# Kernel optimization log

Hardware: AMD Instinct MI355X
Metric: run time of the kernel (lower is better)

Reference implementation:

```python
import jax, jax.numpy as jnp
import numpy as np

B, S, NC, ND, V = 16, 512, 10000, 10000, 128


def _rn(k, shape, scale=0.05):
    return jax.random.normal(k, shape, dtype=jnp.float32) * scale


def setup_inputs() -> dict:
    key = jax.random.key(0)
    ks = jax.random.split(key, 24)
    inp = {
        'c_seq': jax.random.randint(ks[0], (B, S), 0, NC),
        'd_seq': jax.random.randint(ks[1], (B, S), 0, ND),
        'r_seq': jax.random.uniform(ks[2], (B, S), dtype=jnp.float32),
        # embeddings / vectors
        'D1_w': _rn(ks[3], (ND, 1)),
        'D2_w': _rn(ks[4], (ND, V)),
        'v_r': _rn(ks[5], (V,)),
        'v_beta': _rn(ks[6], (V,)),
        # GRU (torch layout: gates ordered r,z,n; W_ih [3V,2V], W_hh [3V,V])
        'W_ih': _rn(ks[7], (3 * V, 2 * V)),
        'W_hh': _rn(ks[8], (3 * V, V)),
        'b_ih': jnp.zeros((3 * V,), jnp.float32),
        'b_hh': jnp.zeros((3 * V,), jnp.float32),
        # linear_1: V -> V -> V -> 1 (weights stored [in, out])
        'm1_W1': _rn(ks[9], (V, V)), 'm1_b1': jnp.zeros((V,), jnp.float32),
        'm1_W2': _rn(ks[10], (V, V)), 'm1_b2': jnp.zeros((V,), jnp.float32),
        'm1_W3': _rn(ks[11], (V, 1)), 'm1_b3': jnp.zeros((1,), jnp.float32),
        # linear_2: 3V -> V -> V -> 1
        'm2_W1': _rn(ks[12], (3 * V, V)), 'm2_b1': jnp.zeros((V,), jnp.float32),
        'm2_W2': _rn(ks[13], (V, V)), 'm2_b2': jnp.zeros((V,), jnp.float32),
        'm2_W3': _rn(ks[14], (V, 1)), 'm2_b3': jnp.zeros((1,), jnp.float32),
    }
    return inp


def _mlp(x, W1, b1, W2, b2, W3, b3):
    h = jax.nn.relu(x @ W1 + b1)
    h = jax.nn.relu(h @ W2 + b2)
    return h @ W3 + b3


def _gru_seq(x, W_ih, W_hh, b_ih, b_hh):
    # x: [B,S,2V] -> h_seq [B,S,V]; torch GRU gate order r,z,n
    xp = x @ W_ih.T + b_ih  # [B,S,3V]

    def step(h, xt):
        hp = h @ W_hh.T + b_hh
        xr, xz, xn = jnp.split(xt, 3, axis=-1)
        hr, hz, hn = jnp.split(hp, 3, axis=-1)
        r = jax.nn.sigmoid(xr + hr)
        z = jax.nn.sigmoid(xz + hz)
        n = jnp.tanh(xn + r * hn)
        h_new = (1.0 - z) * n + z * h
        return h_new, h_new

    h0 = jnp.zeros((x.shape[0], W_hh.shape[1]), x.dtype)
    _, hs = jax.lax.scan(step, h0, jnp.swapaxes(xp, 0, 1))  # [S,B,V]
    return jnp.swapaxes(hs, 0, 1)


def reference(c_seq, d_seq, r_seq, D1_w, D2_w, v_r, v_beta,
              W_ih, W_hh, b_ih, b_hh,
              m1_W1, m1_b1, m1_W2, m1_b2, m1_W3, m1_b3,
              m2_W1, m2_b1, m2_W2, m2_b2, m2_W3, m2_b3):
    v_d_seq = D2_w[d_seq]                     # [B,S,V]
    v_r_seq = r_seq[..., None] * v_r          # [B,S,V]

    h_seq = _gru_seq(jnp.concatenate([v_d_seq, v_r_seq], axis=-1),
                     W_ih, W_hh, b_ih, b_hh)  # [B,S,V]
    alpha_seq = _mlp(h_seq, m1_W1, m1_b1, m1_W2, m1_b2, m1_W3, m1_b3)[..., 0]  # [B,S]

    bidx = jnp.arange(c_seq.shape[0])

    def step(C, ins):
        c_t, vd_t, vr_t = ins                 # [B], [B,V], [B,V]
        beta_prev = C[bidx, c_t]              # gather: [B]
        v_beta_prev = beta_prev[:, None] * v_beta  # [B,V]
        new_c = _mlp(jnp.concatenate([v_beta_prev, vd_t, vr_t], axis=-1),
                     m2_W1, m2_b1, m2_W2, m2_b2, m2_W3, m2_b3)[:, 0]  # [B]
        C = C.at[bidx, c_t].set(new_c)        # scatter
        return C, (C, new_c)

    C0 = jnp.zeros((c_seq.shape[0], NC), jnp.float32)
    _, (C_seq, beta_seq) = jax.lax.scan(
        step, C0,
        (jnp.swapaxes(c_seq, 0, 1), jnp.swapaxes(v_d_seq, 0, 1), jnp.swapaxes(v_r_seq, 0, 1)))
    C_seq = jnp.swapaxes(C_seq, 0, 1)[..., None]   # [B,S,NC,1]
    beta_seq = jnp.swapaxes(beta_seq, 0, 1)        # [B,S]

    gamma_seq = D1_w[d_seq][..., 0]                # [B,S]
    return (alpha_seq, beta_seq, gamma_seq, h_seq, C_seq)
```

## Files before the change

### kernel.cpp

```cpp
#include <hip/hip_runtime.h>

#define Bq   16
#define Sq   512
#define Vq   128
#define NCq  10000

typedef __attribute__((ext_vector_type(8))) short short8v;
typedef __attribute__((ext_vector_type(4))) float f32x4;

#define OFF_P1B_U  3145728u
#define OFF_WTIH   2097152u
#define OFF_WVRIH  2146304u
#define OFF_WVR1   2146688u
#define OFF_WVB    2146816u
#define OFF_PO     2146944u

#define PLN 136
#define PLSZ (16*PLN+8)

__device__ __forceinline__ unsigned short f2bf(float x) {
    unsigned u = __builtin_bit_cast(unsigned, x);
    unsigned r = (u + 0x7fffu + ((u >> 16) & 1u)) >> 16;
    return (unsigned short)r;
}
__device__ __forceinline__ float bfhi(unsigned u) {
    return __builtin_bit_cast(float, u << 16);
}
__device__ __forceinline__ float bflo(unsigned u) {
    return __builtin_bit_cast(float, u & 0xffff0000u);
}
__device__ __forceinline__ void barrier_lgkm() {
    asm volatile("s_waitcnt lgkmcnt(0)" ::: "memory");
    __builtin_amdgcn_sched_barrier(0);
    __builtin_amdgcn_s_barrier();
    __builtin_amdgcn_sched_barrier(0);
}

__global__ __launch_bounds__(256) void k0_prep(
    const int* __restrict__ c_seq, const int* __restrict__ d_seq,
    const float* __restrict__ D1_w,
    const float* __restrict__ W_ih,
    const float* __restrict__ v_r, const float* __restrict__ v_beta,
    const float* __restrict__ m2W1,
    float* __restrict__ ws, float* __restrict__ gamma_out)
{
    const int blk = blockIdx.x, tid = threadIdx.x;

    if (blk < 128) {
        float* WTIH = ws + OFF_WTIH;
        int base = blk * 384;
        for (int i = tid; i < 384; i += 256) {
            int e = base + i;
            int k = e / 384, g = e % 384;
            WTIH[e] = W_ih[g * 256 + k];
        }
    } else if (blk == 128) {
        float* WVRIH = ws + OFF_WVRIH;
        float* WVR1  = ws + OFF_WVR1;
        float* WVB   = ws + OFF_WVB;
        for (int g = tid; g < 384; g += 256) {
            float a = 0.f;
            for (int k = 0; k < 128; ++k) a = fmaf(v_r[k], W_ih[g * 256 + 128 + k], a);
            WVRIH[g] = a;
        }
        if (tid < 128) {
            float a = 0.f, b = 0.f;
            for (int k = 0; k < 128; ++k) {
                a = fmaf(v_r[k],    m2W1[(256 + k) * 128 + tid], a);
                b = fmaf(v_beta[k], m2W1[k * 128 + tid],         b);
            }
            WVR1[tid] = a; WVB[tid] = b;
        }
    } else if (blk < 145) {
        const int b = blk - 129;
        __shared__ int cs[Sq];
        for (int i = tid; i < Sq; i += 256) cs[i] = c_seq[b * Sq + i];
        __syncthreads();
        int* PO = (int*)(ws + OFF_PO);
        for (int t = tid; t < Sq; t += 256) {
            int c = cs[t];
            int po = -1;
            for (int u = t - 1; u >= 0; --u) if (cs[u] == c) { po = u; break; }
            PO[t * 16 + b] = po;
        }
    } else {
        const int b = blk - 145;
        for (int s = tid; s < Sq; s += 256)
            gamma_out[b * Sq + s] = D1_w[d_seq[b * Sq + s]];
    }
}

__global__ __launch_bounds__(256) void k1_gemm(
    const int* __restrict__ d_seq, const float* __restrict__ D2_w,
    const float* __restrict__ m2W1,
    const float* __restrict__ b_ih, const float* __restrict__ b_hh,
    const float* __restrict__ r_seq, const float* __restrict__ m2b1,
    float* __restrict__ ws)
{
    __shared__ float As[64 * 128];
    __shared__ float Bs[128 * 64];
    const int blk = blockIdx.x, tid = threadIdx.x;
    const int nc = blk & 7;
    const int m0 = (blk >> 3) * 64;
    const float* WTIH = ws + OFF_WTIH;

    const float4* D2v = (const float4*)D2_w;
    for (int e = tid; e < 2048; e += 256) {
        int r = e >> 5, q = e & 31;
        int d = d_seq[m0 + r];
        *(float4*)&As[r * 128 + 4 * q] = D2v[d * 32 + q];
    }
    for (int e = tid; e < 2048; e += 256) {
        int k = e >> 4, q = e & 15;
        float4 v;
        if (nc < 6) v = *(const float4*)&WTIH[k * 384 + nc * 64 + 4 * q];
        else        v = *(const float4*)&m2W1[(128 + k) * 128 + (nc - 6) * 64 + 4 * q];
        *(float4*)&Bs[k * 64 + 4 * q] = v;
    }
    __syncthreads();

    const int tx = tid & 15, ty = tid >> 4;
    const int c0 = 4 * tx, r0 = 4 * ty;
    float acc[4][4];
#pragma unroll
    for (int i = 0; i < 4; ++i)
#pragma unroll
        for (int j = 0; j < 4; ++j) acc[i][j] = 0.f;

    for (int k = 0; k < 128; ++k) {
        float4 bv = *(const float4*)&Bs[k * 64 + c0];
#pragma unroll
        for (int i = 0; i < 4; ++i) {
            float a = As[(r0 + i) * 128 + k];
            acc[i][0] = fmaf(a, bv.x, acc[i][0]);
            acc[i][1] = fmaf(a, bv.y, acc[i][1]);
            acc[i][2] = fmaf(a, bv.z, acc[i][2]);
            acc[i][3] = fmaf(a, bv.w, acc[i][3]);
        }
    }

    float rsv[4];
#pragma unroll
    for (int i = 0; i < 4; ++i) rsv[i] = r_seq[m0 + r0 + i];

    if (nc < 6) {
        const int grow0 = nc * 64 + c0;
        float4 bi  = *(const float4*)&b_ih[grow0];
        float4 wv4 = *(const float4*)&(ws + OFF_WVRIH)[grow0];
        float4 bh4 = make_float4(0.f, 0.f, 0.f, 0.f);
        if (nc < 4) bh4 = *(const float4*)&b_hh[grow0];
        unsigned short* XPB = (unsigned short*)ws;
        const int r4 = grow0 >> 2;
#pragma unroll
        for (int i = 0; i < 4; ++i) {
            int row = m0 + r0 + i;
            int t = row & 511, bb = row >> 9;
            float vx = acc[i][0] + bi.x + bh4.x + rsv[i] * wv4.x;
            float vy = acc[i][1] + bi.y + bh4.y + rsv[i] * wv4.y;
            float vz = acc[i][2] + bi.z + bh4.z + rsv[i] * wv4.z;
            float vw = acc[i][3] + bi.w + bh4.w + rsv[i] * wv4.w;
            uint2 p;
            p.x = (unsigned)f2bf(vx) | ((unsigned)f2bf(vy) << 16);
            p.y = (unsigned)f2bf(vz) | ((unsigned)f2bf(vw) << 16);
            *(uint2*)&XPB[((size_t)((bb >> 2) * 512 + t)) * 1536 + r4 * 16 + (bb & 3) * 4] = p;
        }
    } else {
        const int j0 = (nc - 6) * 64 + c0;
        float4 b1v = *(const float4*)&m2b1[j0];
        float4 wr1 = *(const float4*)&(ws + OFF_WVR1)[j0];
        unsigned short* P1B = (unsigned short*)ws + OFF_P1B_U;
#pragma unroll
        for (int i = 0; i < 4; ++i) {
            int row = m0 + r0 + i;
            int t = row & 511, bb = row >> 9;
            float vx = acc[i][0] + b1v.x + rsv[i] * wr1.x;
            float vy = acc[i][1] + b1v.y + rsv[i] * wr1.y;
            float vz = acc[i][2] + b1v.z + rsv[i] * wr1.z;
            float vw = acc[i][3] + b1v.w + rsv[i] * wr1.w;
            uint2 p;
            p.x = (unsigned)f2bf(vx) | ((unsigned)f2bf(vy) << 16);
            p.y = (unsigned)f2bf(vz) | ((unsigned)f2bf(vw) << 16);
            *(uint2*)&P1B[((size_t)(t * 16 + bb)) * 128 + j0] = p;
        }
    }
}

__global__ __launch_bounds__(512, 1) void k2_scan(
    const float* __restrict__ W_hh, const float* __restrict__ b_hh,
    const float* __restrict__ m2W2, const float* __restrict__ m2b2,
    const float* __restrict__ m2W3, const float* __restrict__ m2b3,
    float* __restrict__ ws,
    float* __restrict__ hseq_out, float* __restrict__ beta_out)
{
    __shared__ __align__(16) unsigned char smem[12800];
    const int tid = threadIdx.x;
    const int l = tid & 63, wv = tid >> 6;
    const int qq = l >> 4, cb = l & 15;
    const int bgid = blockIdx.x;

    if (bgid < 4) {
        unsigned short* hP = (unsigned short*)smem;
        const unsigned short* XPB = (const unsigned short*)ws;

        short8v aH0[4], aH1[4], aH2[4];
#pragma unroll
        for (int kf = 0; kf < 4; ++kf) {
            const int kb = kf * 32 + qq * 8;
            const float* w0 = W_hh + (0 * 128 + 16 * wv + cb) * 128 + kb;
            const float* w1 = W_hh + (1 * 128 + 16 * wv + cb) * 128 + kb;
            const float* w2 = W_hh + (2 * 128 + 16 * wv + cb) * 128 + kb;
            short8v h0, h1, h2;
#pragma unroll
            for (int e = 0; e < 8; ++e) {
                h0[e] = (short)f2bf(w0[e]);
                h1[e] = (short)f2bf(w1[e]);
                h2[e] = (short)f2bf(w2[e]);
            }
            aH0[kf] = h0; aH1[kf] = h1; aH2[kf] = h2;
        }
        float bhn[4];
        *(float4*)bhn = *(const float4*)&b_hh[256 + 16 * wv + 4 * qq];

        const size_t pbase = (size_t)(bgid * 512) * 1536 + (4 * wv + qq) * 16 + (cb & 3) * 4;
        uint2 pxA0 = *(const uint2*)(XPB + pbase);
        uint2 pxA1 = *(const uint2*)(XPB + pbase + 512);
        uint2 pxA2 = *(const uint2*)(XPB + pbase + 1024);
        uint2 pxB0 = *(const uint2*)(XPB + pbase + 1536);
        uint2 pxB1 = *(const uint2*)(XPB + pbase + 1536 + 512);
        uint2 pxB2 = *(const uint2*)(XPB + pbase + 1536 + 1024);

        float* hp = hseq_out + ((size_t)((bgid * 4 + (cb & 3)) * 512)) * 128 + 16 * wv + 4 * qq;
        float hold[4] = {0.f, 0.f, 0.f, 0.f};
        for (int i = tid; i < 2 * PLSZ; i += 512) hP[i] = 0;
        __syncthreads();

        for (int t = 0; t < 512; ++t) {
            float pf0[4] = {bfhi(pxA0.x), bflo(pxA0.x), bfhi(pxA0.y), bflo(pxA0.y)};
            float pf1[4] = {bfhi(pxA1.x), bflo(pxA1.x), bfhi(pxA1.y), bflo(pxA1.y)};
            float pf2[4] = {bfhi(pxA2.x), bflo(pxA2.x), bfhi(pxA2.y), bflo(pxA2.y)};
            pxA0 = pxB0; pxA1 = pxB1; pxA2 = pxB2;
            if (t < 510) {
                const unsigned short* s = XPB + pbase + (size_t)(t + 2) * 1536;
                pxB0 = *(const uint2*)(s);
                pxB1 = *(const uint2*)(s + 512);
                pxB2 = *(const uint2*)(s + 1024);
            }
            const unsigned short* HI = hP + (t & 1) * PLSZ;
            unsigned short* HIn = hP + ((t + 1) & 1) * PLSZ;

            f32x4 C0 = {0.f,0.f,0.f,0.f}, C1 = {0.f,0.f,0.f,0.f}, C2 = {0.f,0.f,0.f,0.f};
#pragma unroll
            for (int kf = 0; kf < 4; ++kf) {
                short8v Bh = *(const short8v*)(HI + cb * PLN + kf * 32 + qq * 8);
                C0 = __builtin_amdgcn_mfma_f32_16x16x32_bf16(aH0[kf], Bh, C0, 0, 0, 0);
                C1 = __builtin_amdgcn_mfma_f32_16x16x32_bf16(aH1[kf], Bh, C1, 0, 0, 0);
                C2 = __builtin_amdgcn_mfma_f32_16x16x32_bf16(aH2[kf], Bh, C2, 0, 0, 0);
            }
            float hnew[4];
#pragma unroll
            for (int i = 0; i < 4; ++i) {
                float pr = C0[i] + pf0[i];
                float pz = C1[i] + pf1[i];
                float r = __builtin_amdgcn_rcpf(1.f + __expf(-pr));
                float z = __builtin_amdgcn_rcpf(1.f + __expf(-pz));
                float hn = C2[i] + bhn[i];
                float npre = fmaf(r, hn, pf2[i]);
                float e2 = __expf(-2.f * fabsf(npre));
                float n = copysignf((1.f - e2) * __builtin_amdgcn_rcpf(1.f + e2), npre);
                float hv = fmaf(z, hold[i] - n, n);
                hold[i] = hv;
                hnew[i] = hv;
            }
            if (cb < 4) {
                *(float4*)hp = make_float4(hnew[0], hnew[1], hnew[2], hnew[3]);
                uint2 hw;
                hw.x = (unsigned)f2bf(hnew[0]) | ((unsigned)f2bf(hnew[1]) << 16);
                hw.y = (unsigned)f2bf(hnew[2]) | ((unsigned)f2bf(hnew[3]) << 16);
                *(uint2*)(HIn + cb * PLN + 16 * wv + 4 * qq) = hw;
            }
            hp += 128;
            barrier_lgkm();
        }
    } else {
        const int bq = bgid - 4;
        float* bhL = (float*)smem;
        unsigned short* h1P = (unsigned short*)(smem + 8192);
        float* redT = (float*)(smem + 8192 + 2 * PLSZ);
        const unsigned short* P1B = (const unsigned short*)ws + OFF_P1B_U;
        const int* POg = (const int*)(ws + OFF_PO);

        short8v aH[4];
#pragma unroll
        for (int kf = 0; kf < 4; ++kf) {
            short8v hi;
#pragma unroll
            for (int e = 0; e < 8; ++e)
                hi[e] = (short)f2bf(m2W2[(kf * 32 + qq * 8 + e) * 128 + 16 * wv + cb]);
            aH[kf] = hi;
        }
        float w3C[4], b2C[4];
        *(float4*)w3C = *(const float4*)&m2W3[16 * wv + 4 * qq];
        *(float4*)b2C = *(const float4*)&m2b2[16 * wv + 4 * qq];
        const float b3v = m2b3[0];

        const bool pa = (tid < 128);
        const int bb2 = tid & 3, j4 = (tid >> 2) & 31;
        float wvb[4] = {0.f, 0.f, 0.f, 0.f};
        uint2 p1A = {0, 0}, p1B = {0, 0};
        int poCur = -1, poNxt = -1;
        float bpPre = 0.f, btap = 0.f;
        if (pa) {
            *(float4*)wvb = *(const float4*)&(ws + OFF_WVB)[j4 * 4];
            p1A = *(const uint2*)(P1B + (size_t)(0 * 16 + 4 * bq + bb2) * 128 + j4 * 4);
            p1B = *(const uint2*)(P1B + (size_t)(1 * 16 + 4 * bq + bb2) * 128 + j4 * 4);
            poCur = POg[0 * 16 + 4 * bq + bb2];
            poNxt = POg[1 * 16 + 4 * bq + bb2];
        }
        for (int i = tid; i < PLSZ; i += 512) h1P[i] = 0;
        __syncthreads();

        for (int t = 0; t < 512; ++t) {
            if (pa) {
                float bp = (poCur == t - 1) ? btap : bpPre;
                float f0 = bfhi(p1A.x), f1 = bflo(p1A.x);
                float f2v = bfhi(p1A.y), f3 = bflo(p1A.y);
                float h0 = fmaxf(0.f, fmaf(bp, wvb[0], f0));
                float h1 = fmaxf(0.f, fmaf(bp, wvb[1], f1));
                float h2 = fmaxf(0.f, fmaf(bp, wvb[2], f2v));
                float h3 = fmaxf(0.f, fmaf(bp, wvb[3], f3));
                uint2 hw;
                hw.x = (unsigned)f2bf(h0) | ((unsigned)f2bf(h1) << 16);
                hw.y = (unsigned)f2bf(h2) | ((unsigned)f2bf(h3) << 16);
                *(uint2*)(h1P + bb2 * PLN + j4 * 4) = hw;
                p1A = p1B;
                if (t < 510)
                    p1B = *(const uint2*)(P1B + (size_t)((t + 2) * 16 + 4 * bq + bb2) * 128 + j4 * 4);
            }
            barrier_lgkm();

            if (pa) {
                bpPre = 0.f;
                if (poNxt >= 0 && poNxt < t) bpPre = bhL[bb2 * 512 + poNxt];
                poCur = poNxt;
                if (t < 510) poNxt = POg[(t + 2) * 16 + 4 * bq + bb2];
            }
            f32x4 C = {0.f, 0.f, 0.f, 0.f};
#pragma unroll
            for (int kf = 0; kf < 4; ++kf) {
                short8v Bh = *(const short8v*)(h1P + cb * PLN + kf * 32 + qq * 8);
                C = __builtin_amdgcn_mfma_f32_16x16x32_bf16(aH[kf], Bh, C, 0, 0, 0);
            }
            float part = 0.f;
#pragma unroll
            for (int i = 0; i < 4; ++i)
                part = fmaf(fmaxf(0.f, C[i] + b2C[i]), w3C[i], part);
            part += __shfl_xor(part, 16);
            part += __shfl_xor(part, 32);
            if (qq == 0 && cb < 4) redT[cb * 8 + wv] = part;
            barrier_lgkm();

            if (pa) {
                float4 ra = *(const float4*)&redT[bb2 * 8];
                float4 rb = *(const float4*)&redT[bb2 * 8 + 4];
                float bta = ((ra.x + ra.y) + (ra.z + ra.w)) +
                            ((rb.x + rb.y) + (rb.z + rb.w)) + b3v;
                if (j4 == 0) bhL[bb2 * 512 + t] = bta;
                btap = bta;
            }
        }
        __syncthreads();
        for (int i = tid; i < 2048; i += 512)
            beta_out[(4 * bq + (i >> 9)) * 512 + (i & 511)] = bhL[i];
    }
}

__global__ __launch_bounds__(256) void k2b_fill(
    const int* __restrict__ c_seq, const float* __restrict__ beta_in,
    float* __restrict__ C_out)
{
    __shared__ int   scs[Sq];
    __shared__ float sbt[Sq];
    const int bid = blockIdx.x, tid = threadIdx.x;
    const int b = bid / 40, rem = bid % 40;
    const int chunk = rem >> 2, q = rem & 3;

    for (int i = tid; i < Sq; i += 256) {
        scs[i] = c_seq[b * Sq + i];
        sbt[i] = beta_in[b * Sq + i];
    }
    __syncthreads();

    const int c0 = chunk * 1024 + tid * 4;
    if (c0 >= NCq) return;

    float cur0 = 0.f, cur1 = 0.f, cur2 = 0.f, cur3 = 0.f;
    const int tlo = q * 128, thi = tlo + 128;
    float* base = C_out + (size_t)b * Sq * NCq + c0;

    for (int t = 0; t < tlo; ++t) {
        int ct = scs[t] - c0; float bv = sbt[t];
        cur0 = (ct == 0) ? bv : cur0;
        cur1 = (ct == 1) ? bv : cur1;
        cur2 = (ct == 2) ? bv : cur2;
        cur3 = (ct == 3) ? bv : cur3;
    }
    for (int t = tlo; t < thi; ++t) {
        int ct = scs[t] - c0; float bv = sbt[t];
        cur0 = (ct == 0) ? bv : cur0;
        cur1 = (ct == 1) ? bv : cur1;
        cur2 = (ct == 2) ? bv : cur2;
        cur3 = (ct == 3) ? bv : cur3;
        *(float4*)(base + (size_t)t * NCq) = make_float4(cur0, cur1, cur2, cur3);
    }
}

__global__ __launch_bounds__(256) void k3_alpha(
    const float* __restrict__ hseq,
    const float* __restrict__ W1, const float* __restrict__ b1,
    const float* __restrict__ W2, const float* __restrict__ b2,
    const float* __restrict__ W3, const float* __restrict__ b3,
    float* __restrict__ alpha_out)
{
    __shared__ float Hs[32 * 128];
    __shared__ float T1[32 * 128];
    __shared__ float red[4][16];
    const int blk = blockIdx.x, tid = threadIdx.x;
    const int row0 = blk * 32;

    for (int e = tid; e < 1024; e += 256) {
        int r = e >> 5, q = e & 31;
        *(float4*)&Hs[r * 128 + 4 * q] =
            *(const float4*)&hseq[(size_t)(row0 + r) * 128 + 4 * q];
    }
    __syncthreads();

    const int j = tid & 127, rh = tid >> 7;
    const float b1j = b1[j], b2j = b2[j], w3j = W3[j];
    float acc[16];
#pragma unroll
    for (int r = 0; r < 16; ++r) acc[r] = b1j;
    for (int k = 0; k < 128; ++k) {
        float w = W1[k * 128 + j];
#pragma unroll
        for (int r = 0; r < 16; ++r)
            acc[r] = fmaf(Hs[(rh * 16 + r) * 128 + k], w, acc[r]);
    }
#pragma unroll
    for (int r = 0; r < 16; ++r) {
        acc[r] = fmaxf(acc[r], 0.f);
        T1[(rh * 16 + r) * 128 + j] = acc[r];
    }
    __syncthreads();
    float acc2[16];
#pragma unroll
    for (int r = 0; r < 16; ++r) acc2[r] = b2j;
    for (int k = 0; k < 128; ++k) {
        float w = W2[k * 128 + j];
#pragma unroll
        for (int r = 0; r < 16; ++r)
            acc2[r] = fmaf(T1[(rh * 16 + r) * 128 + k], w, acc2[r]);
    }
#pragma unroll
    for (int r = 0; r < 16; ++r) {
        float p = fmaxf(acc2[r], 0.f) * w3j;
#pragma unroll
        for (int off = 1; off < 64; off <<= 1) p += __shfl_xor(p, off);
        if ((tid & 63) == 0) red[tid >> 6][r] = p;
    }
    __syncthreads();
    if (tid < 32) {
        int rr = tid & 15, g = tid >> 4;
        alpha_out[row0 + g * 16 + rr] = red[2 * g][rr] + red[2 * g + 1][rr] + b3[0];
    }
}

extern "C" void kernel_launch(void* const* d_in, const int* in_sizes, int n_in,
                              void* d_out, int out_size, void* d_ws, size_t ws_size,
                              hipStream_t stream) {
    const int*   c_seq = (const int*)d_in[0];
    const int*   d_seq = (const int*)d_in[1];
    const float* r_seq = (const float*)d_in[2];
    const float* D1_w  = (const float*)d_in[3];
    const float* D2_w  = (const float*)d_in[4];
    const float* v_r   = (const float*)d_in[5];
    const float* v_b   = (const float*)d_in[6];
    const float* W_ih  = (const float*)d_in[7];
    const float* W_hh  = (const float*)d_in[8];
    const float* b_ih  = (const float*)d_in[9];
    const float* b_hh  = (const float*)d_in[10];
    const float* m1W1  = (const float*)d_in[11];
    const float* m1b1  = (const float*)d_in[12];
    const float* m1W2  = (const float*)d_in[13];
    const float* m1b2  = (const float*)d_in[14];
    const float* m1W3  = (const float*)d_in[15];
    const float* m1b3  = (const float*)d_in[16];
    const float* m2W1  = (const float*)d_in[17];
    const float* m2b1  = (const float*)d_in[18];
    const float* m2W2  = (const float*)d_in[19];
    const float* m2b2  = (const float*)d_in[20];
    const float* m2W3  = (const float*)d_in[21];
    const float* m2b3  = (const float*)d_in[22];

    float* out   = (float*)d_out;
    float* alpha = out;
    float* beta  = out + 8192;
    float* gamma = out + 16384;
    float* hseq  = out + 24576;
    float* Cseq  = out + 1073152;
    float* ws    = (float*)d_ws;

    hipLaunchKernelGGL(k0_prep, dim3(161), dim3(256), 0, stream,
                       c_seq, d_seq, D1_w, W_ih, v_r, v_b, m2W1, ws, gamma);
    hipLaunchKernelGGL(k1_gemm, dim3(1024), dim3(256), 0, stream,
                       d_seq, D2_w, m2W1, b_ih, b_hh, r_seq, m2b1, ws);
    hipLaunchKernelGGL(k2_scan, dim3(8), dim3(512), 0, stream,
                       W_hh, b_hh, m2W2, m2b2, m2W3, m2b3, ws, hseq, beta);
    hipLaunchKernelGGL(k2b_fill, dim3(640), dim3(256), 0, stream,
                       c_seq, beta, Cseq);
    hipLaunchKernelGGL(k3_alpha, dim3(256), dim3(256), 0, stream,
                       hseq, m1W1, m1b1, m1W2, m1b2, m1W3, m1b3, alpha);
}
```

Before: 636.6 us.

## Stage scan inputs via async global-to-LDS chunks and split MFMA accumulators

Both sequential scan blocks (GRU and beta MLP) now prefetch their per-step precomputed inputs 8 timesteps at a time, using global_load_lds into double-buffered LDS chunks. Before, each step issued register prefetch loads from global memory. The pointer table is also preloaded into LDS, and the beta reduction is moved to the start of the next step. MFMA accumulation is split into two independent chains to shorten the dependent latency per step. This shortens the serial critical path per timestep at the cost of more LDS use and a periodic vmcnt wait.

```diff
diff --git a/kernel.cpp b/kernel.cpp
--- a/kernel.cpp
+++ b/kernel.cpp
@@ -34,6 +34,15 @@
     __builtin_amdgcn_sched_barrier(0);
     __builtin_amdgcn_s_barrier();
     __builtin_amdgcn_sched_barrier(0);
+}
+__device__ __forceinline__ void wait_vm0() {
+    asm volatile("s_waitcnt vmcnt(0)" ::: "memory");
+    __builtin_amdgcn_sched_barrier(0);
+}
+__device__ __forceinline__ void gload_lds16(const void* g, void* l) {
+    __builtin_amdgcn_global_load_lds(
+        (const __attribute__((address_space(1))) unsigned int*)g,
+        (__attribute__((address_space(3))) unsigned int*)l, 16, 0, 0);
 }
 
 __global__ __launch_bounds__(256) void k0_prep(
@@ -192,14 +201,15 @@
     float* __restrict__ ws,
     float* __restrict__ hseq_out, float* __restrict__ beta_out)
 {
-    __shared__ __align__(16) unsigned char smem[12800];
+    __shared__ __align__(16) unsigned char smem[57984];
     const int tid = threadIdx.x;
     const int l = tid & 63, wv = tid >> 6;
     const int qq = l >> 4, cb = l & 15;
     const int bgid = blockIdx.x;
 
     if (bgid < 4) {
-        unsigned short* hP = (unsigned short*)smem;
+        unsigned short* hP  = (unsigned short*)smem;
+        unsigned short* xch = (unsigned short*)(smem + 8736);
         const unsigned short* XPB = (const unsigned short*)ws;
 
         short8v aH0[4], aH1[4], aH2[4];
@@ -221,50 +231,64 @@
         float bhn[4];
         *(float4*)bhn = *(const float4*)&b_hh[256 + 16 * wv + 4 * qq];
 
-        const size_t pbase = (size_t)(bgid * 512) * 1536 + (4 * wv + qq) * 16 + (cb & 3) * 4;
-        uint2 pxA0 = *(const uint2*)(XPB + pbase);
-        uint2 pxA1 = *(const uint2*)(XPB + pbase + 512);
-        uint2 pxA2 = *(const uint2*)(XPB + pbase + 1024);
-        uint2 pxB0 = *(const uint2*)(XPB + pbase + 1536);
-        uint2 pxB1 = *(const uint2*)(XPB + pbase + 1536 + 512);
-        uint2 pxB2 = *(const uint2*)(XPB + pbase + 1536 + 1024);
-
         float* hp = hseq_out + ((size_t)((bgid * 4 + (cb & 3)) * 512)) * 128 + 16 * wv + 4 * qq;
         float hold[4] = {0.f, 0.f, 0.f, 0.f};
         for (int i = tid; i < 2 * PLSZ; i += 512) hP[i] = 0;
+#pragma unroll
+        for (int rr = 0; rr < 3; ++rr)
+            gload_lds16(XPB + (size_t)(bgid * 512) * 1536 + (rr * 512 + tid) * 8,
+                        xch + (rr * 512 + tid) * 8);
         __syncthreads();
 
         for (int t = 0; t < 512; ++t) {
-            float pf0[4] = {bfhi(pxA0.x), bflo(pxA0.x), bfhi(pxA0.y), bflo(pxA0.y)};
-            float pf1[4] = {bfhi(pxA1.x), bflo(pxA1.x), bfhi(pxA1.y), bflo(pxA1.y)};
-            float pf2[4] = {bfhi(pxA2.x), bflo(pxA2.x), bfhi(pxA2.y), bflo(pxA2.y)};
-            pxA0 = pxB0; pxA1 = pxB1; pxA2 = pxB2;
-            if (t < 510) {
-                const unsigned short* s = XPB + pbase + (size_t)(t + 2) * 1536;
-                pxB0 = *(const uint2*)(s);
-                pxB1 = *(const uint2*)(s + 512);
-                pxB2 = *(const uint2*)(s + 1024);
-            }
+            const int r = t & 7;
+            if (r < 3 && t < 504) {
+                const unsigned short* src =
+                    XPB + (size_t)(bgid * 512 + ((t >> 3) + 1) * 8) * 1536 + (r * 512 + tid) * 8;
+                unsigned short* dst = xch + (((t >> 3) + 1) & 1) * 12288 + (r * 512 + tid) * 8;
+                gload_lds16(src, dst);
+            }
+            const unsigned short* xc =
+                xch + ((t >> 3) & 1) * 12288 + r * 1536 + (4 * wv + qq) * 16 + (cb & 3) * 4;
+            uint2 u0 = *(const uint2*)(xc);
+            uint2 u1 = *(const uint2*)(xc + 512);
+            uint2 u2 = *(const uint2*)(xc + 1024);
+            float pf0[4] = {bfhi(u0.x), bflo(u0.x), bfhi(u0.y), bflo(u0.y)};
+            float pf1[4] = {bfhi(u1.x), bflo(u1.x), bfhi(u1.y), bflo(u1.y)};
+            float pf2[4] = {bfhi(u2.x), bflo(u2.x), bfhi(u2.y), bflo(u2.y)};
+
             const unsigned short* HI = hP + (t & 1) * PLSZ;
             unsigned short* HIn = hP + ((t + 1) & 1) * PLSZ;
 
-            f32x4 C0 = {0.f,0.f,0.f,0.f}, C1 = {0.f,0.f,0.f,0.f}, C2 = {0.f,0.f,0.f,0.f};
-#pragma unroll
-            for (int kf = 0; kf < 4; ++kf) {
-                short8v Bh = *(const short8v*)(HI + cb * PLN + kf * 32 + qq * 8);
-                C0 = __builtin_amdgcn_mfma_f32_16x16x32_bf16(aH0[kf], Bh, C0, 0, 0, 0);
-                C1 = __builtin_amdgcn_mfma_f32_16x16x32_bf16(aH1[kf], Bh, C1, 0, 0, 0);
-                C2 = __builtin_amdgcn_mfma_f32_16x16x32_bf16(aH2[kf], Bh, C2, 0, 0, 0);
+            f32x4 C0a = {0.f,0.f,0.f,0.f}, C1a = {0.f,0.f,0.f,0.f}, C2a = {0.f,0.f,0.f,0.f};
+            f32x4 C0b = {0.f,0.f,0.f,0.f}, C1b = {0.f,0.f,0.f,0.f}, C2b = {0.f,0.f,0.f,0.f};
+            {
+                short8v B0 = *(const short8v*)(HI + cb * PLN + 0 * 32 + qq * 8);
+                short8v B1 = *(const short8v*)(HI + cb * PLN + 1 * 32 + qq * 8);
+                short8v B2 = *(const short8v*)(HI + cb * PLN + 2 * 32 + qq * 8);
+                short8v B3 = *(const short8v*)(HI + cb * PLN + 3 * 32 + qq * 8);
+                C0a = __builtin_amdgcn_mfma_f32_16x16x32_bf16(aH0[0], B0, C0a, 0, 0, 0);
+                C1a = __builtin_amdgcn_mfma_f32_16x16x32_bf16(aH1[0], B0, C1a, 0, 0, 0);
+                C2a = __builtin_amdgcn_mfma_f32_16x16x32_bf16(aH2[0], B0, C2a, 0, 0, 0);
+                C0b = __builtin_amdgcn_mfma_f32_16x16x32_bf16(aH0[1], B1, C0b, 0, 0, 0);
+                C1b = __builtin_amdgcn_mfma_f32_16x16x32_bf16(aH1[1], B1, C1b, 0, 0, 0);
+                C2b = __builtin_amdgcn_mfma_f32_16x16x32_bf16(aH2[1], B1, C2b, 0, 0, 0);
+                C0a = __builtin_amdgcn_mfma_f32_16x16x32_bf16(aH0[2], B2, C0a, 0, 0, 0);
+                C1a = __builtin_amdgcn_mfma_f32_16x16x32_bf16(aH1[2], B2, C1a, 0, 0, 0);
+                C2a = __builtin_amdgcn_mfma_f32_16x16x32_bf16(aH2[2], B2, C2a, 0, 0, 0);
+                C0b = __builtin_amdgcn_mfma_f32_16x16x32_bf16(aH0[3], B3, C0b, 0, 0, 0);
+                C1b = __builtin_amdgcn_mfma_f32_16x16x32_bf16(aH1[3], B3, C1b, 0, 0, 0);
+                C2b = __builtin_amdgcn_mfma_f32_16x16x32_bf16(aH2[3], B3, C2b, 0, 0, 0);
             }
             float hnew[4];
 #pragma unroll
             for (int i = 0; i < 4; ++i) {
-                float pr = C0[i] + pf0[i];
-                float pz = C1[i] + pf1[i];
-                float r = __builtin_amdgcn_rcpf(1.f + __expf(-pr));
+                float pr = (C0a[i] + C0b[i]) + pf0[i];
+                float pz = (C1a[i] + C1b[i]) + pf1[i];
+                float rr2 = __builtin_amdgcn_rcpf(1.f + __expf(-pr));
                 float z = __builtin_amdgcn_rcpf(1.f + __expf(-pz));
-                float hn = C2[i] + bhn[i];
-                float npre = fmaf(r, hn, pf2[i]);
+                float hn = (C2a[i] + C2b[i]) + bhn[i];
+                float npre = fmaf(rr2, hn, pf2[i]);
                 float e2 = __expf(-2.f * fabsf(npre));
                 float n = copysignf((1.f - e2) * __builtin_amdgcn_rcpf(1.f + e2), npre);
                 float hv = fmaf(z, hold[i] - n, n);
@@ -279,13 +303,16 @@
                 *(uint2*)(HIn + cb * PLN + 16 * wv + 4 * qq) = hw;
             }
             hp += 128;
+            if (r == 7) wait_vm0();
             barrier_lgkm();
         }
     } else {
         const int bq = bgid - 4;
         float* bhL = (float*)smem;
-        unsigned short* h1P = (unsigned short*)(smem + 8192);
-        float* redT = (float*)(smem + 8192 + 2 * PLSZ);
+        int*   poT = (int*)(smem + 8192);
+        unsigned short* h1P = (unsigned short*)(smem + 16384);
+        float* redT = (float*)(smem + 20752);
+        unsigned short* pch = (unsigned short*)(smem + 20880);
         const unsigned short* P1B = (const unsigned short*)ws + OFF_P1B_U;
         const int* POg = (const int*)(ws + OFF_PO);
 
@@ -306,67 +333,75 @@
         const bool pa = (tid < 128);
         const int bb2 = tid & 3, j4 = (tid >> 2) & 31;
         float wvb[4] = {0.f, 0.f, 0.f, 0.f};
-        uint2 p1A = {0, 0}, p1B = {0, 0};
-        int poCur = -1, poNxt = -1;
-        float bpPre = 0.f, btap = 0.f;
-        if (pa) {
-            *(float4*)wvb = *(const float4*)&(ws + OFF_WVB)[j4 * 4];
-            p1A = *(const uint2*)(P1B + (size_t)(0 * 16 + 4 * bq + bb2) * 128 + j4 * 4);
-            p1B = *(const uint2*)(P1B + (size_t)(1 * 16 + 4 * bq + bb2) * 128 + j4 * 4);
-            poCur = POg[0 * 16 + 4 * bq + bb2];
-            poNxt = POg[1 * 16 + 4 * bq + bb2];
-        }
+        if (pa) *(float4*)wvb = *(const float4*)&(ws + OFF_WVB)[j4 * 4];
+        float btap = 0.f;
+
+        for (int i = tid; i < 2048; i += 512)
+            poT[i] = POg[(i >> 2) * 16 + 4 * bq + (i & 3)];
         for (int i = tid; i < PLSZ; i += 512) h1P[i] = 0;
+        gload_lds16(P1B + (size_t)(wv * 16 + 4 * bq) * 128 + l * 8,
+                    pch + wv * 512 + l * 8);
         __syncthreads();
 
         for (int t = 0; t < 512; ++t) {
+            const int r = t & 7;
             if (pa) {
-                float bp = (poCur == t - 1) ? btap : bpPre;
-                float f0 = bfhi(p1A.x), f1 = bflo(p1A.x);
-                float f2v = bfhi(p1A.y), f3 = bflo(p1A.y);
-                float h0 = fmaxf(0.f, fmaf(bp, wvb[0], f0));
-                float h1 = fmaxf(0.f, fmaf(bp, wvb[1], f1));
-                float h2 = fmaxf(0.f, fmaf(bp, wvb[2], f2v));
-                float h3 = fmaxf(0.f, fmaf(bp, wvb[3], f3));
+                if (t > 0) {
+                    float4 ra = *(const float4*)&redT[bb2 * 8];
+                    float4 rb = *(const float4*)&redT[bb2 * 8 + 4];
+                    btap = ((ra.x + ra.y) + (ra.z + ra.w)) +
+                           ((rb.x + rb.y) + (rb.z + rb.w)) + b3v;
+                    if (j4 == 0) bhL[bb2 * 512 + (t - 1)] = btap;
+                }
+                int po = poT[t * 4 + bb2];
+                float bp = (po == t - 1) ? btap : ((po >= 0) ? bhL[bb2 * 512 + po] : 0.f);
+                const unsigned short* pc =
+                    pch + ((t >> 3) & 1) * 4096 + r * 512 + bb2 * 128 + j4 * 4;
+                uint2 u = *(const uint2*)pc;
+                float h0 = fmaxf(0.f, fmaf(bp, wvb[0], bfhi(u.x)));
+                float h1 = fmaxf(0.f, fmaf(bp, wvb[1], bflo(u.x)));
+                float h2 = fmaxf(0.f, fmaf(bp, wvb[2], bfhi(u.y)));
+                float h3 = fmaxf(0.f, fmaf(bp, wvb[3], bflo(u.y)));
                 uint2 hw;
                 hw.x = (unsigned)f2bf(h0) | ((unsigned)f2bf(h1) << 16);
                 hw.y = (unsigned)f2bf(h2) | ((unsigned)f2bf(h3) << 16);
                 *(uint2*)(h1P + bb2 * PLN + j4 * 4) = hw;
-                p1A = p1B;
-                if (t < 510)
-                    p1B = *(const uint2*)(P1B + (size_t)((t + 2) * 16 + 4 * bq + bb2) * 128 + j4 * 4);
+            }
+            if (r == 0 && t < 504) {
+                const unsigned short* src =
+                    P1B + (size_t)((t + 8 + wv) * 16 + 4 * bq) * 128 + l * 8;
+                unsigned short* dst = pch + (((t >> 3) + 1) & 1) * 4096 + wv * 512 + l * 8;
+                gload_lds16(src, dst);
             }
             barrier_lgkm();
 
-            if (pa) {
-                bpPre = 0.f;
-                if (poNxt >= 0 && poNxt < t) bpPre = bhL[bb2 * 512 + poNxt];
-                poCur = poNxt;
-                if (t < 510) poNxt = POg[(t + 2) * 16 + 4 * bq + bb2];
-            }
-            f32x4 C = {0.f, 0.f, 0.f, 0.f};
-#pragma unroll
-            for (int kf = 0; kf < 4; ++kf) {
-                short8v Bh = *(const short8v*)(h1P + cb * PLN + kf * 32 + qq * 8);
-                C = __builtin_amdgcn_mfma_f32_16x16x32_bf16(aH[kf], Bh, C, 0, 0, 0);
+            f32x4 Ca = {0.f, 0.f, 0.f, 0.f}, Cb = {0.f, 0.f, 0.f, 0.f};
+            {
+                short8v B0 = *(const short8v*)(h1P + cb * PLN + 0 * 32 + qq * 8);
+                short8v B1 = *(const short8v*)(h1P + cb * PLN + 1 * 32 + qq * 8);
+                short8v B2 = *(const short8v*)(h1P + cb * PLN + 2 * 32 + qq * 8);
+                short8v B3 = *(const short8v*)(h1P + cb * PLN + 3 * 32 + qq * 8);
+                Ca = __builtin_amdgcn_mfma_f32_16x16x32_bf16(aH[0], B0, Ca, 0, 0, 0);
+                Cb = __builtin_amdgcn_mfma_f32_16x16x32_bf16(aH[1], B1, Cb, 0, 0, 0);
+                Ca = __builtin_amdgcn_mfma_f32_16x16x32_bf16(aH[2], B2, Ca, 0, 0, 0);
+                Cb = __builtin_amdgcn_mfma_f32_16x16x32_bf16(aH[3], B3, Cb, 0, 0, 0);
             }
             float part = 0.f;
 #pragma unroll
             for (int i = 0; i < 4; ++i)
-                part = fmaf(fmaxf(0.f, C[i] + b2C[i]), w3C[i], part);
+                part = fmaf(fmaxf(0.f, (Ca[i] + Cb[i]) + b2C[i]), w3C[i], part);
             part += __shfl_xor(part, 16);
             part += __shfl_xor(part, 32);
             if (qq == 0 && cb < 4) redT[cb * 8 + wv] = part;
+            if (r == 7) wait_vm0();
             barrier_lgkm();
-
-            if (pa) {
-                float4 ra = *(const float4*)&redT[bb2 * 8];
-                float4 rb = *(const float4*)&redT[bb2 * 8 + 4];
-                float bta = ((ra.x + ra.y) + (ra.z + ra.w)) +
-                            ((rb.x + rb.y) + (rb.z + rb.w)) + b3v;
-                if (j4 == 0) bhL[bb2 * 512 + t] = bta;
-                btap = bta;
-            }
+        }
+        if (pa) {
+            float4 ra = *(const float4*)&redT[bb2 * 8];
+            float4 rb = *(const float4*)&redT[bb2 * 8 + 4];
+            float bta = ((ra.x + ra.y) + (ra.z + ra.w)) +
+                        ((rb.x + rb.y) + (rb.z + rb.w)) + b3v;
+            if (j4 == 0) bhL[bb2 * 512 + 511] = bta;
         }
         __syncthreads();
         for (int i = tid; i < 2048; i += 512)
```

Result: no change. 630.4 us (-1.0%).
